# Kernel tuning notes

Hardware: AMD Instinct MI355X
Metric: run time of the kernel (lower is better)

## Reference

```python
import jax, jax.numpy as jnp
import numpy as np

B, J, L = 32, 16, 4096
MU_P = 0.15
MASK_ID = 103
VOCAB = 30522


def setup_inputs() -> dict:
    key = jax.random.key(0)
    k1, k2, k3 = jax.random.split(key, 3)
    input_ids = jax.random.randint(k1, (B, J, L), 0, VOCAB, dtype=jnp.int64 if jax.config.jax_enable_x64 else jnp.int32)
    # first half: nonnegative per-token weights; second half: shared-token ids (unused by the math)
    my_attention_mask = jax.random.uniform(k2, (B, J, 2 * L), dtype=jnp.float32)
    # uniform noise for Gumbel keys (weighted sampling w/o replacement)
    u = jax.random.uniform(k3, (B, J, L), dtype=jnp.float32, minval=1e-6, maxval=1.0)
    return {"input_ids": input_ids, "my_attention_mask": my_attention_mask, "u": u}


def reference(input_ids, my_attention_mask, u):
    # Split the mask: first half holds sampling weights (second half is unused).
    Lh = my_attention_mask.shape[-1] // 2
    w = my_attention_mask[..., :Lh]                       # [B, J, L]
    nz = w > 0                                            # valid positions
    cnt = nz.sum(axis=-1)                                 # [B, J] number of nonzero weights
    num_to_mask = jnp.floor(MU_P * cnt.astype(w.dtype)).astype(jnp.int32)  # int(mu_p * len)

    # Gumbel-key trick == weighted permutation without replacement over nonzero positions.
    g = -jnp.log(-jnp.log(u))
    scores = jnp.where(nz, jnp.log(jnp.maximum(w, 1e-30)) + g, -jnp.inf)
    # rank of each position in descending-score order
    rank = jnp.argsort(jnp.argsort(-scores, axis=-1), axis=-1)
    sel = (rank < num_to_mask[..., None]) & nz            # [B, J, L] positions to mask

    out_mask = sel.astype(w.dtype)
    out_ids = jnp.where(sel, jnp.asarray(MASK_ID, dtype=input_ids.dtype), input_ids)
    return out_ids, out_mask, -out_mask
```

## Files before the change

### kernel.cpp

```cpp
#include <hip/hip_runtime.h>

#define L_LEN 4096
#define NT 512
#define ROWS 512
#define SLOP 48u
#define BCAP 256

__global__ __launch_bounds__(NT) void AttentionEssentialReinforce_51238959841470_kernel(
    const int* __restrict__ ids,
    const float* __restrict__ amask,
    const float* __restrict__ uin,
    float* __restrict__ out,
    int n_per)
{
    __shared__ unsigned int hist[4096];
    __shared__ unsigned int s_wtot[8], s_woff[8];
    __shared__ unsigned long long bkey[BCAP];
    __shared__ int bidx[BCAP];
    __shared__ unsigned int s_cnt, s_or, s_remk, s_prefix, s_nhi, s_bn;

    const int row = blockIdx.x;
    const int tid = threadIdx.x;
    const int lane = tid & 63, wid = tid >> 6;
    const float* wrow = amask + (size_t)row * (2 * L_LEN);
    const float* urow = uin + (size_t)row * L_LEN;

    if (tid == 0) { s_cnt = 0; s_or = 0; s_nhi = 0; s_bn = 0; }
    __syncthreads();

    if (((const unsigned*)ids)[2 * tid + 1] != 0u) s_or = 1u;

    float wv[8], uv[8];
    {
        float4 a0 = reinterpret_cast<const float4*>(wrow)[tid];
        float4 a1 = reinterpret_cast<const float4*>(wrow)[NT + tid];
        float4 b0 = reinterpret_cast<const float4*>(urow)[tid];
        float4 b1 = reinterpret_cast<const float4*>(urow)[NT + tid];
        wv[0]=a0.x; wv[1]=a0.y; wv[2]=a0.z; wv[3]=a0.w;
        wv[4]=a1.x; wv[5]=a1.y; wv[6]=a1.z; wv[7]=a1.w;
        uv[0]=b0.x; uv[1]=b0.y; uv[2]=b0.z; uv[3]=b0.w;
        uv[4]=b1.x; uv[5]=b1.y; uv[6]=b1.z; uv[7]=b1.w;
    }
    unsigned key[8];
    unsigned localnz = 0;
    #pragma unroll
    for (int e = 0; e < 8; ++e) {
        key[e] = 0u;
        if (wv[e] > 0.0f) {
            float t = -logf(uv[e]);
            float r = fmaxf(wv[e], 1e-30f) / t;
            key[e] = __float_as_uint(r);
            localnz++;
        }
    }
    unsigned v = localnz;
    #pragma unroll
    for (int off = 32; off > 0; off >>= 1) v += __shfl_down(v, off, 64);
    if (lane == 0) atomicAdd(&s_cnt, v);
    __syncthreads();

    const bool is64 = (s_or == 0u);
    const int cnt = (int)s_cnt;
    const int k = (int)floorf(0.15f * (float)cnt);

    int ida[8];
    if (!is64) {
        const int4* idr = reinterpret_cast<const int4*>(ids + (size_t)row * L_LEN);
        int4 t0 = idr[tid], t1 = idr[NT + tid];
        ida[0]=t0.x; ida[1]=t0.y; ida[2]=t0.z; ida[3]=t0.w;
        ida[4]=t1.x; ida[5]=t1.y; ida[6]=t1.z; ida[7]=t1.w;
    } else {
        const longlong2* idr = reinterpret_cast<const longlong2*>(
            (const long long*)ids + (size_t)row * L_LEN);
        longlong2 a = idr[2 * tid], b = idr[2 * tid + 1];
        longlong2 c = idr[2 * (NT + tid)], d = idr[2 * (NT + tid) + 1];
        ida[0]=(int)a.x; ida[1]=(int)a.y; ida[2]=(int)b.x; ida[3]=(int)b.y;
        ida[4]=(int)c.x; ida[5]=(int)c.y; ida[6]=(int)d.x; ida[7]=(int)d.y;
    }

    unsigned lo_thr = 0xFFFFFFFFu, hi_thr = 0xFFFFFFFFu;
    int need = 0;
    unsigned bn = 0;

    if (k > 0) {
        for (int b = tid; b < 4096; b += NT) hist[b] = 0;
        __syncthreads();
        #pragma unroll
        for (int e = 0; e < 8; ++e) atomicAdd(&hist[key[e] >> 20], 1u);
        __syncthreads();
        {
            int b0 = 4095 - 8 * tid;
            unsigned c[8], lsum = 0;
            #pragma unroll
            for (int m = 0; m < 8; ++m) { c[m] = hist[b0 - m]; lsum += c[m]; }
            unsigned scan = lsum;
            #pragma unroll
            for (int off = 1; off < 64; off <<= 1) {
                unsigned o = __shfl_up(scan, (unsigned)off, 64);
                if (lane >= off) scan += o;
            }
            if (lane == 63) s_wtot[wid] = scan;
            __syncthreads();
            if (tid < 8) {
                unsigned acc = 0;
                for (int w2 = 0; w2 < tid; ++w2) acc += s_wtot[w2];
                s_woff[tid] = acc;
            }
            __syncthreads();
            unsigned run = s_woff[wid] + (scan - lsum);
            unsigned remk = (unsigned)k;
            #pragma unroll
            for (int m = 0; m < 8; ++m) {
                if (run < remk && run + c[m] >= remk) {
                    s_prefix = (unsigned)(b0 - m);
                    s_remk = remk - run;
                }
                run += c[m];
            }
        }
        __syncthreads();
        unsigned prefix12 = s_prefix;
        unsigned remk = s_remk;

        if (tid < 256) hist[tid] = 0;
        __syncthreads();
        #pragma unroll
        for (int e = 0; e < 8; ++e)
            if ((key[e] >> 20) == prefix12)
                atomicAdd(&hist[(key[e] >> 12) & 0xFFu], 1u);
        __syncthreads();
        if (tid < 64) {
            unsigned c[4], lsum = 0;
            #pragma unroll
            for (int m = 0; m < 4; ++m) { c[m] = hist[255 - 4 * tid - m]; lsum += c[m]; }
            unsigned scan = lsum;
            #pragma unroll
            for (int off = 1; off < 64; off <<= 1) {
                unsigned o = __shfl_up(scan, (unsigned)off, 64);
                if (tid >= off) scan += o;
            }
            unsigned run = scan - lsum;
            #pragma unroll
            for (int m = 0; m < 4; ++m) {
                if (run < remk && run + c[m] >= remk) {
                    s_prefix = (prefix12 << 8) | (unsigned)(255 - 4 * tid - m);
                }
                run += c[m];
            }
        }
        __syncthreads();
        const unsigned T20 = s_prefix;
        const unsigned B_lo = T20 << 12, B_hi = (T20 << 12) | 0xFFFu;

        lo_thr = (B_lo > SLOP) ? B_lo - SLOP : 1u;
        hi_thr = B_hi + SLOP;
        unsigned nhi = 0;
        #pragma unroll
        for (int e = 0; e < 8; ++e) {
            if (key[e] > hi_thr) {
                nhi++;
            } else if (key[e] >= lo_thr) {
                unsigned pos = atomicAdd(&s_bn, 1u);
                if (pos < BCAP) {
                    double t = -log((double)uv[e]);
                    double r = (double)fmaxf(wv[e], 1e-30f) / t;
                    bkey[pos] = (unsigned long long)__double_as_longlong(r);
                    bidx[pos] = 4 * ((e >> 2) * NT + tid) + (e & 3);
                }
            }
        }
        unsigned nv = nhi;
        #pragma unroll
        for (int off = 32; off > 0; off >>= 1) nv += __shfl_down(nv, off, 64);
        if (lane == 0) atomicAdd(&s_nhi, nv);
        __syncthreads();
        need = k - (int)s_nhi;
        bn = s_bn; if (bn > BCAP) bn = BCAP;
    }

    const size_t obase = (size_t)row * L_LEN;
    float* o0 = out + obase;
    float* o1 = out + (size_t)n_per + obase;
    float* o2 = out + 2 * (size_t)n_per + obase;

    float f0[8], f1[8], f2[8];
    #pragma unroll
    for (int e = 0; e < 8; ++e) {
        bool sel;
        if (key[e] > hi_thr) {
            sel = true;
        } else if (key[e] < lo_thr) {
            sel = false;
        } else {
            double t = -log((double)uv[e]);
            double r = (double)fmaxf(wv[e], 1e-30f) / t;
            unsigned long long myk = (unsigned long long)__double_as_longlong(r);
            int myi = 4 * ((e >> 2) * NT + tid) + (e & 3);
            int rnk = 0;
            for (unsigned j = 0; j < bn; ++j)
                rnk += (bkey[j] > myk) || (bkey[j] == myk && bidx[j] < myi);
            sel = (rnk < need);
        }
        f0[e] = sel ? 103.0f : (float)ida[e];
        f1[e] = sel ? 1.0f : 0.0f;
        f2[e] = sel ? -1.0f : -0.0f;
    }
    reinterpret_cast<float4*>(o0)[tid]      = make_float4(f0[0], f0[1], f0[2], f0[3]);
    reinterpret_cast<float4*>(o0)[NT + tid] = make_float4(f0[4], f0[5], f0[6], f0[7]);
    reinterpret_cast<float4*>(o1)[tid]      = make_float4(f1[0], f1[1], f1[2], f1[3]);
    reinterpret_cast<float4*>(o1)[NT + tid] = make_float4(f1[4], f1[5], f1[6], f1[7]);
    reinterpret_cast<float4*>(o2)[tid]      = make_float4(f2[0], f2[1], f2[2], f2[3]);
    reinterpret_cast<float4*>(o2)[NT + tid] = make_float4(f2[4], f2[5], f2[6], f2[7]);
}

extern "C" void kernel_launch(void* const* d_in, const int* in_sizes, int n_in,
                              void* d_out, int out_size, void* d_ws, size_t ws_size,
                              hipStream_t stream) {
    const int*   ids   = (const int*)d_in[0];
    const float* amask = (const float*)d_in[1];
    const float* uin   = (const float*)d_in[2];
    float* out = (float*)d_out;

    const int n_per = ROWS * L_LEN;

    AttentionEssentialReinforce_51238959841470_kernel<<<dim3(ROWS), dim3(NT), 0, stream>>>(
        ids, amask, uin, out, n_per);
}
```

Measured before the change: 87.18 us.

## Derive nonzero count from histogram and skip second radix pass when bucket small

Builds the 12-bit key histogram in the first pass (nonzero keys only) and takes the nonzero count from the scan total, which removes the separate count reduction and a barrier. The histogram is zeroed with vector stores alongside the input loads. When the selected coarse bucket holds at most BSKIP elements, the second 8-bit refinement pass is skipped and the whole bucket goes to the exact candidate list. BCAP is doubled to allow this, so the per-element rank loop over candidates can become longer and more shared memory is used.

```diff
diff --git a/kernel.cpp b/kernel.cpp
--- a/kernel.cpp
+++ b/kernel.cpp
@@ -4,7 +4,8 @@
 #define NT 512
 #define ROWS 512
 #define SLOP 48u
-#define BCAP 256
+#define BCAP 512
+#define BSKIP (BCAP - 64)
 
 __global__ __launch_bounds__(NT) void AttentionEssentialReinforce_51238959841470_kernel(
     const int* __restrict__ ids,
@@ -17,7 +18,7 @@
     __shared__ unsigned int s_wtot[8], s_woff[8];
     __shared__ unsigned long long bkey[BCAP];
     __shared__ int bidx[BCAP];
-    __shared__ unsigned int s_cnt, s_or, s_remk, s_prefix, s_nhi, s_bn;
+    __shared__ unsigned int s_or, s_prefix, s_remk, s_csel, s_nhi, s_bn;
 
     const int row = blockIdx.x;
     const int tid = threadIdx.x;
@@ -25,24 +26,23 @@
     const float* wrow = amask + (size_t)row * (2 * L_LEN);
     const float* urow = uin + (size_t)row * L_LEN;
 
-    if (tid == 0) { s_cnt = 0; s_or = 0; s_nhi = 0; s_bn = 0; }
-    __syncthreads();
-
+    float4 a0 = reinterpret_cast<const float4*>(wrow)[tid];
+    float4 a1 = reinterpret_cast<const float4*>(wrow)[NT + tid];
+    float4 b0 = reinterpret_cast<const float4*>(urow)[tid];
+    float4 b1 = reinterpret_cast<const float4*>(urow)[NT + tid];
+
+    if (tid == 0) { s_or = 0; s_nhi = 0; s_bn = 0; }
+    {
+        uint4 z = make_uint4(0, 0, 0, 0);
+        reinterpret_cast<uint4*>(hist)[tid] = z;
+        reinterpret_cast<uint4*>(hist)[NT + tid] = z;
+    }
     if (((const unsigned*)ids)[2 * tid + 1] != 0u) s_or = 1u;
-
-    float wv[8], uv[8];
-    {
-        float4 a0 = reinterpret_cast<const float4*>(wrow)[tid];
-        float4 a1 = reinterpret_cast<const float4*>(wrow)[NT + tid];
-        float4 b0 = reinterpret_cast<const float4*>(urow)[tid];
-        float4 b1 = reinterpret_cast<const float4*>(urow)[NT + tid];
-        wv[0]=a0.x; wv[1]=a0.y; wv[2]=a0.z; wv[3]=a0.w;
-        wv[4]=a1.x; wv[5]=a1.y; wv[6]=a1.z; wv[7]=a1.w;
-        uv[0]=b0.x; uv[1]=b0.y; uv[2]=b0.z; uv[3]=b0.w;
-        uv[4]=b1.x; uv[5]=b1.y; uv[6]=b1.z; uv[7]=b1.w;
-    }
+    __syncthreads();
+
+    float wv[8] = {a0.x, a0.y, a0.z, a0.w, a1.x, a1.y, a1.z, a1.w};
+    float uv[8] = {b0.x, b0.y, b0.z, b0.w, b1.x, b1.y, b1.z, b1.w};
     unsigned key[8];
-    unsigned localnz = 0;
     #pragma unroll
     for (int e = 0; e < 8; ++e) {
         key[e] = 0u;
@@ -50,19 +50,10 @@
             float t = -logf(uv[e]);
             float r = fmaxf(wv[e], 1e-30f) / t;
             key[e] = __float_as_uint(r);
-            localnz++;
-        }
-    }
-    unsigned v = localnz;
-    #pragma unroll
-    for (int off = 32; off > 0; off >>= 1) v += __shfl_down(v, off, 64);
-    if (lane == 0) atomicAdd(&s_cnt, v);
-    __syncthreads();
-
+            atomicAdd(&hist[key[e] >> 20], 1u);
+        }
+    }
     const bool is64 = (s_or == 0u);
-    const int cnt = (int)s_cnt;
-    const int k = (int)floorf(0.15f * (float)cnt);
-
     int ida[8];
     if (!is64) {
         const int4* idr = reinterpret_cast<const int4*>(ids + (size_t)row * L_LEN);
@@ -77,83 +68,90 @@
         ida[0]=(int)a.x; ida[1]=(int)a.y; ida[2]=(int)b.x; ida[3]=(int)b.y;
         ida[4]=(int)c.x; ida[5]=(int)c.y; ida[6]=(int)d.x; ida[7]=(int)d.y;
     }
+    __syncthreads();
+
+    int b0i = 4095 - 8 * tid;
+    unsigned c[8], lsum = 0;
+    #pragma unroll
+    for (int m = 0; m < 8; ++m) { c[m] = hist[b0i - m]; lsum += c[m]; }
+    unsigned scan = lsum;
+    #pragma unroll
+    for (int off = 1; off < 64; off <<= 1) {
+        unsigned o = __shfl_up(scan, (unsigned)off, 64);
+        if (lane >= off) scan += o;
+    }
+    if (lane == 63) s_wtot[wid] = scan;
+    __syncthreads();
+    if (tid < 8) {
+        unsigned acc = 0;
+        for (int w2 = 0; w2 < tid; ++w2) acc += s_wtot[w2];
+        s_woff[tid] = acc;
+    }
+    __syncthreads();
+
+    const int cnt = (int)(s_woff[7] + s_wtot[7]);
+    const int k = (int)floorf(0.15f * (float)cnt);
 
     unsigned lo_thr = 0xFFFFFFFFu, hi_thr = 0xFFFFFFFFu;
     int need = 0;
     unsigned bn = 0;
 
     if (k > 0) {
-        for (int b = tid; b < 4096; b += NT) hist[b] = 0;
-        __syncthreads();
+        unsigned run = s_woff[wid] + (scan - lsum);
+        unsigned remk = (unsigned)k;
         #pragma unroll
-        for (int e = 0; e < 8; ++e) atomicAdd(&hist[key[e] >> 20], 1u);
-        __syncthreads();
-        {
-            int b0 = 4095 - 8 * tid;
-            unsigned c[8], lsum = 0;
+        for (int m = 0; m < 8; ++m) {
+            if (run < remk && run + c[m] >= remk) {
+                s_prefix = (unsigned)(b0i - m);
+                s_remk = remk - run;
+                s_csel = c[m];
+            }
+            run += c[m];
+        }
+    }
+    __syncthreads();
+
+    if (k > 0) {
+        unsigned T12 = s_prefix, remk = s_remk, csel = s_csel;
+        unsigned B_lo, B_hi;
+        if (csel <= BSKIP) {
+            B_lo = T12 << 20;
+            B_hi = (T12 << 20) | 0xFFFFFu;
+        } else {
+            if (tid < 256) hist[tid] = 0;
+            __syncthreads();
             #pragma unroll
-            for (int m = 0; m < 8; ++m) { c[m] = hist[b0 - m]; lsum += c[m]; }
-            unsigned scan = lsum;
-            #pragma unroll
-            for (int off = 1; off < 64; off <<= 1) {
-                unsigned o = __shfl_up(scan, (unsigned)off, 64);
-                if (lane >= off) scan += o;
-            }
-            if (lane == 63) s_wtot[wid] = scan;
+            for (int e = 0; e < 8; ++e)
+                if ((key[e] >> 20) == T12)
+                    atomicAdd(&hist[(key[e] >> 12) & 0xFFu], 1u);
             __syncthreads();
-            if (tid < 8) {
-                unsigned acc = 0;
-                for (int w2 = 0; w2 < tid; ++w2) acc += s_wtot[w2];
-                s_woff[tid] = acc;
+            if (tid < 64) {
+                unsigned cc[4], ls = 0;
+                #pragma unroll
+                for (int m = 0; m < 4; ++m) { cc[m] = hist[255 - 4 * tid - m]; ls += cc[m]; }
+                unsigned sc = ls;
+                #pragma unroll
+                for (int off = 1; off < 64; off <<= 1) {
+                    unsigned o = __shfl_up(sc, (unsigned)off, 64);
+                    if (tid >= off) sc += o;
+                }
+                unsigned rn = sc - ls;
+                #pragma unroll
+                for (int m = 0; m < 4; ++m) {
+                    if (rn < remk && rn + cc[m] >= remk)
+                        s_prefix = (T12 << 8) | (unsigned)(255 - 4 * tid - m);
+                    rn += cc[m];
+                }
             }
             __syncthreads();
-            unsigned run = s_woff[wid] + (scan - lsum);
-            unsigned remk = (unsigned)k;
-            #pragma unroll
-            for (int m = 0; m < 8; ++m) {
-                if (run < remk && run + c[m] >= remk) {
-                    s_prefix = (unsigned)(b0 - m);
-                    s_remk = remk - run;
-                }
-                run += c[m];
-            }
-        }
-        __syncthreads();
-        unsigned prefix12 = s_prefix;
-        unsigned remk = s_remk;
-
-        if (tid < 256) hist[tid] = 0;
-        __syncthreads();
-        #pragma unroll
-        for (int e = 0; e < 8; ++e)
-            if ((key[e] >> 20) == prefix12)
-                atomicAdd(&hist[(key[e] >> 12) & 0xFFu], 1u);
-        __syncthreads();
-        if (tid < 64) {
-            unsigned c[4], lsum = 0;
-            #pragma unroll
-            for (int m = 0; m < 4; ++m) { c[m] = hist[255 - 4 * tid - m]; lsum += c[m]; }
-            unsigned scan = lsum;
-            #pragma unroll
-            for (int off = 1; off < 64; off <<= 1) {
-                unsigned o = __shfl_up(scan, (unsigned)off, 64);
-                if (tid >= off) scan += o;
-            }
-            unsigned run = scan - lsum;
-            #pragma unroll
-            for (int m = 0; m < 4; ++m) {
-                if (run < remk && run + c[m] >= remk) {
-                    s_prefix = (prefix12 << 8) | (unsigned)(255 - 4 * tid - m);
-                }
-                run += c[m];
-            }
-        }
-        __syncthreads();
-        const unsigned T20 = s_prefix;
-        const unsigned B_lo = T20 << 12, B_hi = (T20 << 12) | 0xFFFu;
+            unsigned T20 = s_prefix;
+            B_lo = T20 << 12;
+            B_hi = (T20 << 12) | 0xFFFu;
+        }
 
         lo_thr = (B_lo > SLOP) ? B_lo - SLOP : 1u;
         hi_thr = B_hi + SLOP;
+
         unsigned nhi = 0;
         #pragma unroll
         for (int e = 0; e < 8; ++e) {
@@ -173,7 +171,10 @@
         #pragma unroll
         for (int off = 32; off > 0; off >>= 1) nv += __shfl_down(nv, off, 64);
         if (lane == 0) atomicAdd(&s_nhi, nv);
-        __syncthreads();
+    }
+    __syncthreads();
+
+    if (k > 0) {
         need = k - (int)s_nhi;
         bn = s_bn; if (bn > BCAP) bn = BCAP;
     }
```

After: 133.0 us. 1.53x slower.
